# Kernel optimization log

Hardware: AMD Instinct MI355X
Metric: run time of the kernel (lower is better)

The kernel has to match this reference:

```python
import jax, jax.numpy as jnp
import numpy as np

N = 50000      # nodes
IN = 128       # in_dim
HID = 128      # hidden_dim
HEADS = 4
OUT = HID // HEADS   # per-head out_channels
R = 8          # num_relations
E = 640000     # message-passing edges
E2 = 200000    # decode edge pairs
NC = 8         # num_classes
EPS_LN = 1e-5


def layer_norm(x, g, b):
    m = x.mean(-1, keepdims=True)
    v = ((x - m) ** 2).mean(-1, keepdims=True)
    return (x - m) * jax.lax.rsqrt(v + EPS_LN) * g + b


def rgat_conv(x, edge_index, edge_type, W, q, k, b):
    # PyG RGATConv defaults: additive-self-attention, across-relation softmax,
    # concat=True, negative_slope=0.2, sum aggregation.
    src, dst = edge_index[0], edge_index[1]
    # relation-specific transform for all nodes, then gather per edge
    xw = jnp.einsum('ni,rio->nro', x, W)          # [N, R, HID]
    xi = xw[dst, edge_type]                        # [E, HID] target feats
    xj = xw[src, edge_type]                        # [E, HID] source feats
    alpha = jax.nn.leaky_relu(xi @ q + xj @ k, negative_slope=0.2)  # [E, HEADS]
    # softmax over incoming edges of each destination node (per head)
    amax = jax.ops.segment_max(alpha, dst, num_segments=N)
    amax = jnp.where(jnp.isfinite(amax), amax, 0.0)
    ex = jnp.exp(alpha - amax[dst])
    den = jax.ops.segment_sum(ex, dst, num_segments=N)
    attn = ex / (den[dst] + 1e-16)                 # [E, HEADS]
    msg = (xj.reshape(E, HEADS, OUT) * attn[:, :, None]).reshape(E, HID)
    out = jax.ops.segment_sum(msg, dst, num_segments=N)  # [N, HID]
    return out + b


def setup_inputs() -> dict:
    key = jax.random.key(0)
    ks = jax.random.split(key, 12)
    sI = 1.0 / np.sqrt(IN)
    sH = 1.0 / np.sqrt(HID)
    return {
        'x': jax.random.normal(ks[0], (N, IN), jnp.float32),
        'edge_index': jax.random.randint(ks[1], (2, E), 0, N),
        'edge_type': jax.random.randint(ks[2], (E,), 0, R),
        'edges': jax.random.randint(ks[3], (E2, 2), 0, N),
        'w1': jax.random.normal(ks[4], (R, IN, HID), jnp.float32) * sI,
        'q1': jax.random.normal(ks[5], (HID, HEADS), jnp.float32) * sH,
        'k1': jax.random.normal(ks[6], (HID, HEADS), jnp.float32) * sH,
        'b1': jnp.zeros((HID,), jnp.float32),
        'w2': jax.random.normal(ks[7], (R, HID, HID), jnp.float32) * sH,
        'q2': jax.random.normal(ks[8], (HID, HEADS), jnp.float32) * sH,
        'k2': jax.random.normal(ks[9], (HID, HEADS), jnp.float32) * sH,
        'b2': jnp.zeros((HID,), jnp.float32),
        'ln1_g': jnp.ones((HID,), jnp.float32),
        'ln1_b': jnp.zeros((HID,), jnp.float32),
        'ln2_g': jnp.ones((HID,), jnp.float32),
        'ln2_b': jnp.zeros((HID,), jnp.float32),
        'mw1': jax.random.normal(ks[10], (2 * HID, HID), jnp.float32) / np.sqrt(2 * HID),
        'mb1': jnp.zeros((HID,), jnp.float32),
        'mw2': jax.random.normal(ks[11], (HID, NC), jnp.float32) * sH,
        'mb2': jnp.zeros((NC,), jnp.float32),
    }


def reference(x, edge_index, edge_type, edges,
              w1, q1, k1, b1, w2, q2, k2, b2,
              ln1_g, ln1_b, ln2_g, ln2_b,
              mw1, mb1, mw2, mb2):
    # encode (dropout is identity in eval mode)
    h1 = rgat_conv(x, edge_index, edge_type, w1, q1, k1, b1)
    h1 = layer_norm(jax.nn.relu(h1), ln1_g, ln1_b)
    h2 = rgat_conv(h1, edge_index, edge_type, w2, q2, k2, b2)
    h2 = layer_norm(jax.nn.relu(h2), ln2_g, ln2_b)
    h = h1 + h2
    # decode: gather node pairs, concat, MLP
    z = jnp.concatenate([h[edges[:, 0]], h[edges[:, 1]]], axis=1)  # [E2, 2*HID]
    z = jax.nn.gelu(z @ mw1 + mb1, approximate=False)
    return z @ mw2 + mb2  # [E2, NC]
```

## Files before the change

### kernel.cpp

```cpp
#include <hip/hip_runtime.h>
#include <hip/hip_bf16.h>

#define NN    50000
#define RR    8
#define HIDC  128
#define NHEADS 4
#define EE    640000
#define EE2   200000
#define NCL   8

typedef __hip_bfloat16 bf16;
typedef unsigned short u16;
typedef __attribute__((ext_vector_type(8))) short short8;
typedef __attribute__((ext_vector_type(4))) float floatx4;

__device__ __forceinline__ float us2f(u16 u) {
    return __uint_as_float(((unsigned)u) << 16);
}
__device__ __forceinline__ float bf2f(bf16 v) { return __bfloat162float(v); }
__device__ __forceinline__ u16 f2us(float f) {
    bf16 h = __float2bfloat16(f);
    return *(u16*)&h;
}
__device__ __forceinline__ float ldf(const void* p, int i, bool f32) {
    return f32 ? ((const float*)p)[i] : us2f(((const u16*)p)[i]);
}

__global__ __launch_bounds__(1024) void k_zs(const u16* __restrict__ x,
                                             int* __restrict__ flags,
                                             int* __restrict__ p) {
    if (blockIdx.x < 49) {
        int i = blockIdx.x * 1024 + threadIdx.x;
        if (i < NN) p[i] = 0;
        return;
    }
    __shared__ int cnt;
    if (threadIdx.x == 0) cnt = 0;
    __syncthreads();
    int c = 0;
#pragma unroll
    for (int it = 0; it < 8; it++) {
        ushort4 a = ((const ushort4*)x)[(it * 1024 + threadIdx.x) * 2];
        ushort4 b = ((const ushort4*)x)[(it * 1024 + threadIdx.x) * 2 + 1];
        c += (((a.x >> 7) & 0xFF) == 0xFF) + (((a.y >> 7) & 0xFF) == 0xFF)
           + (((a.z >> 7) & 0xFF) == 0xFF) + (((a.w >> 7) & 0xFF) == 0xFF)
           + (((b.x >> 7) & 0xFF) == 0xFF) + (((b.y >> 7) & 0xFF) == 0xFF)
           + (((b.z >> 7) & 0xFF) == 0xFF) + (((b.w >> 7) & 0xFF) == 0xFF);
    }
    c += __shfl_xor(c, 32); c += __shfl_xor(c, 16); c += __shfl_xor(c, 8);
    c += __shfl_xor(c, 4);  c += __shfl_xor(c, 2);  c += __shfl_xor(c, 1);
    if ((threadIdx.x & 63) == 0) atomicAdd(&cnt, c);
    __syncthreads();
    if (threadIdx.x == 0) { flags[0] = (cnt > 16) ? 1 : 0; flags[1] = 0; }
}

__global__ void k_hist(const int* __restrict__ ei, int* __restrict__ deg) {
    int e = blockIdx.x * 256 + threadIdx.x;
    if (e < EE) atomicAdd(&deg[ei[EE + e]], 1);
}

__global__ __launch_bounds__(256) void k_s1q(const int* __restrict__ deg,
                                             int* __restrict__ bsum,
                                             const void* __restrict__ w1, const void* __restrict__ w2,
                                             const void* __restrict__ q1, const void* __restrict__ k1,
                                             const void* __restrict__ q2, const void* __restrict__ k2,
                                             float* __restrict__ qkw, const int* __restrict__ fl) {
    if (blockIdx.x < 196) {
        int i = blockIdx.x * 256 + threadIdx.x;
        int v = (i < NN) ? deg[i] : 0;
        __shared__ int red[4];
        int lane = threadIdx.x & 63, w = threadIdx.x >> 6;
#pragma unroll
        for (int off = 32; off; off >>= 1) v += __shfl_xor(v, off);
        if (lane == 0) red[w] = v;
        __syncthreads();
        if (threadIdx.x == 0) bsum[blockIdx.x] = red[0] + red[1] + red[2] + red[3];
        return;
    }
    int idx = (blockIdx.x - 196) * 256 + threadIdx.x;
    const bool f = fl[0] != 0;
    int mat = idx >> 10;
    int i   = (idx >> 3) & 127;
    int h8  = idx & 7;
    const void* W = (mat >= 8) ? w2 : w1;
    const void* qk = (mat >= 8) ? ((h8 < 4) ? q2 : k2) : ((h8 < 4) ? q1 : k1);
    int h = h8 & 3;
    int r = mat & 7;
    float acc = 0.f;
    for (int o = 0; o < HIDC; o++)
        acc += ldf(W, (r * HIDC + i) * HIDC + o, f) * ldf(qk, o * NHEADS + h, f);
    qkw[idx] = acc;
}

__global__ __launch_bounds__(256) void k_scan2(const int* __restrict__ bsum,
                                               int* __restrict__ boff,
                                               int* __restrict__ rowptr) {
    __shared__ int s[256];
    int t = threadIdx.x;
    s[t] = (t < 196) ? bsum[t] : 0;
    __syncthreads();
    for (int off = 1; off < 256; off <<= 1) {
        int u = (t >= off) ? s[t - off] : 0;
        __syncthreads();
        s[t] += u;
        __syncthreads();
    }
    if (t < 196) boff[t] = (t == 0) ? 0 : s[t - 1];
    if (t == 255) rowptr[NN] = s[255];
}

__global__ __launch_bounds__(256) void k_s3w(int* __restrict__ deg ,
                                             const int* __restrict__ boff,
                                             int* __restrict__ rowptr,
                                             const void* __restrict__ w1, const void* __restrict__ w2,
                                             const float* __restrict__ qkw,
                                             u16* __restrict__ Wf2, const int* __restrict__ fl) {
    if (blockIdx.x < 196) {
        __shared__ int s[256];
        int t = threadIdx.x;
        int i = blockIdx.x * 256 + t;
        int v = (i < NN) ? deg[i] : 0;
        s[t] = v;
        __syncthreads();
        for (int off = 1; off < 256; off <<= 1) {
            int u = (t >= off) ? s[t - off] : 0;
            __syncthreads();
            s[t] += u;
            __syncthreads();
        }
        if (i < NN) {
            int val = boff[blockIdx.x] + s[t] - v;
            rowptr[i] = val;
            deg[i] = val;
        }
        return;
    }
    int idx = (blockIdx.x - 196) * 256 + threadIdx.x;
    const bool f = fl[0] != 0;
    int mat = idx / 2304, rest = idx % 2304;
    int c = rest >> 8, q = (rest >> 6) & 3, ln = rest & 63;
    int k0 = q * 32 + (ln >> 4) * 8;
    int nn = c * 16 + (ln & 15);
    int r = mat & 7;
    u16 o[8];
    if (c < 8) {
        const void* W = (mat >= 8) ? w2 : w1;
#pragma unroll
        for (int j = 0; j < 8; j++)
            o[j] = f2us(ldf(W, (r * HIDC + k0 + j) * HIDC + nn, f));
    } else {
        int col = nn - 128;
#pragma unroll
        for (int j = 0; j < 8; j++)
            o[j] = (col < 8) ? f2us(qkw[mat * 1024 + (k0 + j) * 8 + col]) : (u16)0;
    }
    u16* dst = Wf2 + (size_t)mat * 18432 + (size_t)(((c * 4 + q) * 64 + ln) * 8);
    *(ushort4*)dst       = ushort4{o[0], o[1], o[2], o[3]};
    *(ushort4*)(dst + 4) = ushort4{o[4], o[5], o[6], o[7]};
}

__global__ void k_scatter(const int* __restrict__ ei, const int* __restrict__ et,
                          int* __restrict__ cursor, int* __restrict__ elist) {
    int e = blockIdx.x * 256 + threadIdx.x;
    if (e >= EE) return;
    int pos = atomicAdd(&cursor[ei[EE + e]], 1);
    elist[pos] = ei[e] * RR + et[e];
}

__global__ __launch_bounds__(512) void k_xw2(const void* __restrict__ X,
                                             const u16* __restrict__ Wf2,
                                             bf16* __restrict__ xw,
                                             float* __restrict__ sbuf,
                                             float* __restrict__ tbuf,
                                             const int* __restrict__ fx,
                                             int layer) {
    __shared__ u16 U[8 * 16 * 136];
    u16* Xs = U;
    const int tid = threadIdx.x;
    const int n0 = blockIdx.x * 64;
    const bool xf = fx[0] != 0;
    for (int v = tid; v < 2048; v += 512) {
        int row = v >> 5, c4 = (v & 31) * 4, n = n0 + row;
        ushort4 o = {0, 0, 0, 0};
        if (n < NN) {
            if (xf) {
                float4 hv = *(const float4*)((const float*)X + (size_t)n * HIDC + c4);
                o = ushort4{f2us(hv.x), f2us(hv.y), f2us(hv.z), f2us(hv.w)};
            } else {
                o = *(const ushort4*)((const u16*)X + (size_t)n * HIDC + c4);
            }
        }
        *(ushort4*)&Xs[row * 136 + c4] = o;
    }
    __syncthreads();
    const int w = tid >> 6, lane = tid & 63;
    const int wr = w & 3;
    const int rh = w >> 2;
    short8 af[4];
#pragma unroll
    for (int q = 0; q < 4; q++)
        af[q] = *(const short8*)&Xs[(16 * wr + (lane & 15)) * 136 + q * 32 + (lane >> 4) * 8];
    __syncthreads();
    u16* Ow = U + w * 2176;
    for (int rr = 0; rr < 4; rr++) {
        const int r = rh * 4 + rr;
        const u16* Wfr = Wf2 + (size_t)(layer * 8 + r) * 18432;
#pragma unroll
        for (int c = 0; c < 9; c++) {
            floatx4 acc = {0.f, 0.f, 0.f, 0.f};
#pragma unroll
            for (int q = 0; q < 4; q++) {
                short8 bfr = *(const short8*)&Wfr[(size_t)(((c * 4 + q) * 64 + lane) * 8)];
                acc = __builtin_amdgcn_mfma_f32_16x16x32_bf16(af[q], bfr, acc, 0, 0, 0);
            }
            if (c < 8) {
                int col = c * 16 + (lane & 15);
#pragma unroll
                for (int reg = 0; reg < 4; reg++) {
                    int lp = (lane >> 4) * 4 + reg;
                    Ow[lp * 136 + col] = f2us(acc[reg]);
                }
            } else {
                int cl = lane & 15;
                if (cl < 8) {
                    float* dstp = (cl < 4) ? sbuf : tbuf;
                    int h = cl & 3;
#pragma unroll
                    for (int reg = 0; reg < 4; reg++) {
                        int p = 16 * wr + (lane >> 4) * 4 + reg;
                        int n = n0 + p;
                        if (n < NN) dstp[(size_t)(n * RR + r) * 4 + h] = acc[reg];
                    }
                }
            }
        }
#pragma unroll
        for (int i = 0; i < 4; i++) {
            int v = i * 64 + lane;
            int lrow = v >> 4;
            int c8 = (v & 15) * 8;
            int n = n0 + 16 * wr + lrow;
            if (n < NN) {
                short8 hv = *(const short8*)&Ow[lrow * 136 + c8];
                *(short8*)((u16*)xw + (size_t)(n * RR + r) * HIDC + c8) = hv;
            }
        }
    }
}

__global__ __launch_bounds__(256) void k_score(const int* __restrict__ rowptr,
                                               const int* __restrict__ srlist,
                                               const float* __restrict__ sb,
                                               const float* __restrict__ tb,
                                               float* __restrict__ abuf,
                                               float* __restrict__ linv) {
    __shared__ float sbs[16][8][4];
    const int tid = threadIdx.x;
    const int grp = tid >> 4, sl = tid & 15;
    const int d = blockIdx.x * 16 + grp;
    const int start = rowptr[d], end = rowptr[d + 1];
    if (sl < 8)
        *(float4*)&sbs[grp][sl][0] = *(const float4*)&sb[(size_t)(d * RR + sl) * 4];
    const int nE = end - start;
    float m0 = -1e30f, m1 = -1e30f, m2 = -1e30f, m3 = -1e30f;
    float l0 = 0.f, l1 = 0.f, l2 = 0.f, l3 = 0.f;
    if (nE <= 16) {
        float a0, a1, a2, a3;
        if (sl < nE) {
            int sr = srlist[start + sl];
            int r = sr & 7;
            float4 tj = *(const float4*)&tb[(size_t)sr * 4];
            a0 = sbs[grp][r][0] + tj.x; a0 = a0 >= 0.f ? a0 : 0.2f * a0;
            a1 = sbs[grp][r][1] + tj.y; a1 = a1 >= 0.f ? a1 : 0.2f * a1;
            a2 = sbs[grp][r][2] + tj.z; a2 = a2 >= 0.f ? a2 : 0.2f * a2;
            a3 = sbs[grp][r][3] + tj.w; a3 = a3 >= 0.f ? a3 : 0.2f * a3;
        } else { a0 = a1 = a2 = a3 = -1e30f; }
        float c0m = a0, c1m = a1, c2m = a2, c3m = a3;
#pragma unroll
        for (int off = 8; off; off >>= 1) {
            c0m = fmaxf(c0m, __shfl_xor(c0m, off));
            c1m = fmaxf(c1m, __shfl_xor(c1m, off));
            c2m = fmaxf(c2m, __shfl_xor(c2m, off));
            c3m = fmaxf(c3m, __shfl_xor(c3m, off));
        }
        m0 = fmaxf(c0m, -1e30f); m1 = c1m; m2 = c2m; m3 = c3m;
        float e0 = 0.f, e1 = 0.f, e2 = 0.f, e3 = 0.f;
        if (sl < nE) {
            e0 = __expf(a0 - m0); e1 = __expf(a1 - m1);
            e2 = __expf(a2 - m2); e3 = __expf(a3 - m3);
            *(float4*)&abuf[(size_t)(start + sl) * 4] = float4{e0, e1, e2, e3};
        }
        l0 = e0; l1 = e1; l2 = e2; l3 = e3;
#pragma unroll
        for (int off = 8; off; off >>= 1) {
            l0 += __shfl_xor(l0, off);
            l1 += __shfl_xor(l1, off);
            l2 += __shfl_xor(l2, off);
            l3 += __shfl_xor(l3, off);
        }
    } else {
        for (int c0 = start; c0 < end; c0 += 16) {
            int n = end - c0; if (n > 16) n = 16;
            float a0, a1, a2, a3;
            if (sl < n) {
                int sr = srlist[c0 + sl];
                int r = sr & 7;
                float4 tj = *(const float4*)&tb[(size_t)sr * 4];
                a0 = sbs[grp][r][0] + tj.x; a0 = a0 >= 0.f ? a0 : 0.2f * a0;
                a1 = sbs[grp][r][1] + tj.y; a1 = a1 >= 0.f ? a1 : 0.2f * a1;
                a2 = sbs[grp][r][2] + tj.z; a2 = a2 >= 0.f ? a2 : 0.2f * a2;
                a3 = sbs[grp][r][3] + tj.w; a3 = a3 >= 0.f ? a3 : 0.2f * a3;
                *(float4*)&abuf[(size_t)(c0 + sl) * 4] = float4{a0, a1, a2, a3};
            } else { a0 = a1 = a2 = a3 = -1e30f; }
            m0 = fmaxf(m0, a0); m1 = fmaxf(m1, a1);
            m2 = fmaxf(m2, a2); m3 = fmaxf(m3, a3);
        }
#pragma unroll
        for (int off = 8; off; off >>= 1) {
            m0 = fmaxf(m0, __shfl_xor(m0, off));
            m1 = fmaxf(m1, __shfl_xor(m1, off));
            m2 = fmaxf(m2, __shfl_xor(m2, off));
            m3 = fmaxf(m3, __shfl_xor(m3, off));
        }
        for (int c0 = start; c0 < end; c0 += 16) {
            int n = end - c0; if (n > 16) n = 16;
            float e0 = 0.f, e1 = 0.f, e2 = 0.f, e3 = 0.f;
            if (sl < n) {
                float4 a = *(const float4*)&abuf[(size_t)(c0 + sl) * 4];
                e0 = __expf(a.x - m0); e1 = __expf(a.y - m1);
                e2 = __expf(a.z - m2); e3 = __expf(a.w - m3);
                *(float4*)&abuf[(size_t)(c0 + sl) * 4] = float4{e0, e1, e2, e3};
            }
            l0 += e0; l1 += e1; l2 += e2; l3 += e3;
        }
#pragma unroll
        for (int off = 8; off; off >>= 1) {
            l0 += __shfl_xor(l0, off);
            l1 += __shfl_xor(l1, off);
            l2 += __shfl_xor(l2, off);
            l3 += __shfl_xor(l3, off);
        }
    }
    if (sl == 0) {
        *(float4*)&linv[(size_t)d * 4] =
            float4{1.f / (l0 + 1e-16f), 1.f / (l1 + 1e-16f),
                   1.f / (l2 + 1e-16f), 1.f / (l3 + 1e-16f)};
    }
}

__global__ __launch_bounds__(256) void k_agg(const int* __restrict__ rowptr,
                                             const int* __restrict__ srlist,
                                             const float* __restrict__ abuf,
                                             const float* __restrict__ linvb,
                                             const bf16* __restrict__ xw,
                                             const void* __restrict__ b,
                                             const void* __restrict__ g,
                                             const void* __restrict__ bb,
                                             const u16* __restrict__ hprev,
                                             u16* __restrict__ hout,
                                             const int* __restrict__ fl) {
    __shared__ int   srs[16][16];
    __shared__ float exs[16][17][4];
    const int tid = threadIdx.x;
    const int grp = tid >> 4;
    const int sl  = tid & 15;
    const int hh  = sl >> 2;
    const int d   = blockIdx.x * 16 + grp;
    const bool f = fl[0] != 0;
    const int start = rowptr[d], end = rowptr[d + 1];
    float acc[8];
#pragma unroll
    for (int i = 0; i < 8; i++) acc[i] = 0.f;
    for (int c0 = start; c0 < end; c0 += 16) {
        int n = end - c0;
        if (n > 16) n = 16;
        int sr = 0;
        float4 e4 = {0.f, 0.f, 0.f, 0.f};
        if (sl < n) {
            sr = srlist[c0 + sl];
            e4 = *(const float4*)&abuf[(size_t)(c0 + sl) * 4];
        }
        srs[grp][sl] = sr;
        *(float4*)&exs[grp][sl][0] = e4;
        {
            short8 u[8]; float wv[8];
#pragma unroll
            for (int t = 0; t < 8; t++) {
                int s = srs[grp][t];
                wv[t] = exs[grp][t][hh];
                u[t] = *(const short8*)((const u16*)xw + (size_t)s * HIDC + sl * 8);
            }
#pragma unroll
            for (int t = 0; t < 8; t++)
#pragma unroll
                for (int i = 0; i < 8; i++) acc[i] += wv[t] * us2f((u16)u[t][i]);
        }
        if (n > 8) {
            short8 u[8]; float wv[8];
#pragma unroll
            for (int t = 0; t < 8; t++) {
                int s = srs[grp][8 + t];
                wv[t] = exs[grp][8 + t][hh];
                u[t] = *(const short8*)((const u16*)xw + (size_t)s * HIDC + sl * 8);
            }
#pragma unroll
            for (int t = 0; t < 8; t++)
#pragma unroll
                for (int i = 0; i < 8; i++) acc[i] += wv[t] * us2f((u16)u[t][i]);
        }
    }
    float inv = linvb[(size_t)d * 4 + hh];
    float v[8];
#pragma unroll
    for (int i = 0; i < 8; i++)
        v[i] = fmaxf(acc[i] * inv + ldf(b, sl * 8 + i, f), 0.f);
    float sum = 0.f;
#pragma unroll
    for (int i = 0; i < 8; i++) sum += v[i];
#pragma unroll
    for (int off = 8; off; off >>= 1) sum += __shfl_xor(sum, off);
    float mean = sum * (1.f / 128.f);
    float sq = 0.f;
#pragma unroll
    for (int i = 0; i < 8; i++) { v[i] -= mean; sq += v[i] * v[i]; }
#pragma unroll
    for (int off = 8; off; off >>= 1) sq += __shfl_xor(sq, off);
    float rstd = rsqrtf(sq * (1.f / 128.f) + 1e-5f);
    short8 o;
#pragma unroll
    for (int i = 0; i < 8; i++) {
        float y = v[i] * rstd * ldf(g, sl * 8 + i, f) + ldf(bb, sl * 8 + i, f);
        o[i] = (short)f2us(y);
    }
    if (hprev) {
        short8 hv = *(const short8*)&hprev[(size_t)d * HIDC + sl * 8];
#pragma unroll
        for (int i = 0; i < 8; i++)
            o[i] = (short)f2us(us2f((u16)o[i]) + us2f((u16)hv[i]));
    }
    *(short8*)&hout[(size_t)d * HIDC + sl * 8] = o;
}

__global__ void k_dswz(const void* __restrict__ mw1, const void* __restrict__ mw2,
                       u16* __restrict__ Wf, const int* __restrict__ fl) {
    int idx = blockIdx.x * 256 + threadIdx.x;
    if (idx >= 4352) return;
    const bool f = fl[0] != 0;
    u16 o[8];
    if (idx < 4096) {
        int c = idx >> 9, q = (idx >> 6) & 7, ln = idx & 63;
        int k0 = q * 32 + (ln >> 4) * 8;
        int nn = c * 16 + (ln & 15);
#pragma unroll
        for (int j = 0; j < 8; j++)
            o[j] = f2us(ldf(mw1, (k0 + j) * HIDC + nn, f));
    } else {
        int fidx = idx - 4096;
        int q = fidx >> 6, ln = fidx & 63;
        int k0 = q * 32 + (ln >> 4) * 8;
        int nn = ln & 15;
#pragma unroll
        for (int j = 0; j < 8; j++)
            o[j] = (nn < 8) ? f2us(ldf(mw2, (k0 + j) * NCL + nn, f)) : (u16)0;
    }
    *(ushort4*)&Wf[idx * 8]     = ushort4{o[0], o[1], o[2], o[3]};
    *(ushort4*)&Wf[idx * 8 + 4] = ushort4{o[4], o[5], o[6], o[7]};
}

__global__ __launch_bounds__(256) void k_decode2(const u16* __restrict__ h,
                                                 const int* __restrict__ edges,
                                                 const u16* __restrict__ Wf,
                                                 const void* __restrict__ mb1,
                                                 const void* __restrict__ mb2,
                                                 void* __restrict__ out,
                                                 const int* __restrict__ fl) {
    __shared__ u16 zsu[64 * 136];
    const int tid = threadIdx.x;
    const bool f = fl[0] != 0;
    const int p0 = blockIdx.x * 64;
    const int w = tid >> 6, lane = tid & 63;
    const int m = 16 * w + (lane & 15);
    const int g = lane >> 4;
    const int na = edges[(size_t)(p0 + m) * 2];
    const int nb = edges[(size_t)(p0 + m) * 2 + 1];
    short8 af[8];
#pragma unroll
    for (int q = 0; q < 8; q++) {
        int k0 = q * 32 + g * 8;
        af[q] = *(const short8*)(h + (size_t)((k0 >> 7) ? nb : na) * HIDC + (k0 & 127));
    }
#pragma unroll
    for (int c = 0; c < 8; c++) {
        floatx4 acc = {0.f, 0.f, 0.f, 0.f};
#pragma unroll
        for (int q = 0; q < 8; q++) {
            short8 bfr = *(const short8*)&Wf[(size_t)(((c * 8 + q) * 64 + lane) * 8)];
            acc = __builtin_amdgcn_mfma_f32_16x16x32_bf16(af[q], bfr, acc, 0, 0, 0);
        }
        int col = c * 16 + (lane & 15);
        float bv = ldf(mb1, col, f);
#pragma unroll
        for (int reg = 0; reg < 4; reg++) {
            int p = 16 * w + (lane >> 4) * 4 + reg;
            float z = acc[reg] + bv;
            zsu[p * 136 + col] = f2us(0.5f * z * (1.f + erff(z * 0.70710678118654752f)));
        }
    }
    floatx4 acc2 = {0.f, 0.f, 0.f, 0.f};
#pragma unroll
    for (int q = 0; q < 4; q++) {
        short8 af2 = *(const short8*)&zsu[m * 136 + q * 32 + g * 8];
        short8 bfr2 = *(const short8*)&Wf[32768 + (size_t)((q * 64 + lane) * 8)];
        acc2 = __builtin_amdgcn_mfma_f32_16x16x32_bf16(af2, bfr2, acc2, 0, 0, 0);
    }
    int col16 = lane & 15;
    if (col16 < 8) {
        float bv2 = ldf(mb2, col16, f);
#pragma unroll
        for (int reg = 0; reg < 4; reg++) {
            int p = 16 * w + (lane >> 4) * 4 + reg;
            float sv = acc2[reg] + bv2;
            size_t oi = (size_t)(p0 + p) * NCL + col16;
            if (f) ((float*)out)[oi] = sv;
            else   ((bf16*)out)[oi] = __float2bfloat16(sv);
        }
    }
}

extern "C" void kernel_launch(void* const* d_in, const int* in_sizes, int n_in,
                              void* d_out, int out_size, void* d_ws, size_t ws_size,
                              hipStream_t stream) {
    (void)in_sizes; (void)n_in; (void)out_size; (void)ws_size;
    const void* x    = d_in[0];
    const int* ei    = (const int*)d_in[1];
    const int* et    = (const int*)d_in[2];
    const int* edges = (const int*)d_in[3];
    const void* w1 = d_in[4];
    const void* q1 = d_in[5];
    const void* k1 = d_in[6];
    const void* b1 = d_in[7];
    const void* w2 = d_in[8];
    const void* q2 = d_in[9];
    const void* k2 = d_in[10];
    const void* b2 = d_in[11];
    const void* ln1g = d_in[12];
    const void* ln1b = d_in[13];
    const void* ln2g = d_in[14];
    const void* ln2b = d_in[15];
    const void* mw1 = d_in[16];
    const void* mb1 = d_in[17];
    const void* mw2 = d_in[18];
    const void* mb2 = d_in[19];

    char* ws = (char*)d_ws;
    bf16* xwb   = (bf16*)ws;
    u16* Wf     = (u16*)ws;
    float* sbuf = (float*)(ws + 102400000);
    float* tbuf = (float*)(ws + 108800000);
    u16* h1     = (u16*)(ws + 115200000);
    float* abuf = (float*)(ws + 128000000);
    float* linv = (float*)(ws + 138240000);
    int* bsum   = (int*)(ws + 139040000);
    int* boff   = (int*)(ws + 139041024);
    u16* hsum   = (u16*)(ws + 140800000);
    u16* Wf2    = (u16*)(ws + 153600000);
    int* rowptr = (int*)(ws + 166400000);
    int* cursor = (int*)(ws + 166600016);
    int* elist  = (int*)(ws + 166800016);
    float* qkw  = (float*)(ws + 169360016);
    int* flags  = (int*)(ws + 169425552);

    k_zs<<<50, 1024, 0, stream>>>((const u16*)x, flags, cursor);
    k_hist<<<2500, 256, 0, stream>>>(ei, cursor);
    k_s1q<<<260, 256, 0, stream>>>(cursor, bsum, w1, w2, q1, k1, q2, k2, qkw, flags);
    k_scan2<<<1, 256, 0, stream>>>(bsum, boff, rowptr);
    k_s3w<<<340, 256, 0, stream>>>(cursor, boff, rowptr, w1, w2, qkw, Wf2, flags);
    k_scatter<<<2500, 256, 0, stream>>>(ei, et, cursor, elist);

    for (int layer = 0; layer < 2; ++layer) {
        const void* b  = layer ? b2 : b1;
        const void* lg = layer ? ln2g : ln1g;
        const void* lb = layer ? ln2b : ln1b;
        k_xw2<<<782, 512, 0, stream>>>(layer ? (const void*)h1 : x, Wf2, xwb,
                                       sbuf, tbuf,
                                       layer ? flags + 1 : flags, layer);
        k_score<<<3125, 256, 0, stream>>>(rowptr, elist, sbuf, tbuf, abuf, linv);
        k_agg<<<3125, 256, 0, stream>>>(rowptr, elist, abuf, linv, xwb,
                                        b, lg, lb,
                                        layer ? h1 : (const u16*)nullptr,
                                        layer ? hsum : h1, flags);
    }
    k_dswz<<<17, 256, 0, stream>>>(mw1, mw2, Wf, flags);
    k_decode2<<<3125, 256, 0, stream>>>(hsum, edges, Wf, mb1, mb2, d_out, flags);
}
```

Baseline: 469.2 us.

## Aggregate raw features per relation then apply W via MFMA in aggregation

Stops materialising the per-node, per-relation transformed features xw ([N,R,HID] in bf16). Edges are now bucketed by (destination, relation), and the aggregation kernel sums attention-weighted raw source features for each relation and head. It then multiplies each per-relation sum by W_r with MFMA inside the same kernel. The projection kernel now computes only the attention score projections and writes a bf16 copy of x. This removes the large xw write and its scattered reads, at the cost of a larger 400k-entry CSR and scan, per-relation serial edge loops, and eight MFMA passes with barriers per block.

New measurement: 540.1 us. 15.1% more time.

```diff
diff --git a/kernel.cpp b/kernel.cpp
--- a/kernel.cpp
+++ b/kernel.cpp
@@ -8,6 +8,8 @@
 #define EE    640000
 #define EE2   200000
 #define NCL   8
+#define NB2   400000
+#define SB2   1563
 
 typedef __hip_bfloat16 bf16;
 typedef unsigned short u16;
@@ -17,7 +19,6 @@
 __device__ __forceinline__ float us2f(u16 u) {
     return __uint_as_float(((unsigned)u) << 16);
 }
-__device__ __forceinline__ float bf2f(bf16 v) { return __bfloat162float(v); }
 __device__ __forceinline__ u16 f2us(float f) {
     bf16 h = __float2bfloat16(f);
     return *(u16*)&h;
@@ -29,9 +30,9 @@
 __global__ __launch_bounds__(1024) void k_zs(const u16* __restrict__ x,
                                              int* __restrict__ flags,
                                              int* __restrict__ p) {
-    if (blockIdx.x < 49) {
+    if (blockIdx.x < 391) {
         int i = blockIdx.x * 1024 + threadIdx.x;
-        if (i < NN) p[i] = 0;
+        if (i < NB2) p[i] = 0;
         return;
     }
     __shared__ int cnt;
@@ -54,9 +55,10 @@
     if (threadIdx.x == 0) { flags[0] = (cnt > 16) ? 1 : 0; flags[1] = 0; }
 }
 
-__global__ void k_hist(const int* __restrict__ ei, int* __restrict__ deg) {
+__global__ void k_hist(const int* __restrict__ ei, const int* __restrict__ et,
+                       int* __restrict__ deg) {
     int e = blockIdx.x * 256 + threadIdx.x;
-    if (e < EE) atomicAdd(&deg[ei[EE + e]], 1);
+    if (e < EE) atomicAdd(&deg[ei[EE + e] * RR + et[e]], 1);
 }
 
 __global__ __launch_bounds__(256) void k_s1q(const int* __restrict__ deg,
@@ -65,9 +67,9 @@
                                              const void* __restrict__ q1, const void* __restrict__ k1,
                                              const void* __restrict__ q2, const void* __restrict__ k2,
                                              float* __restrict__ qkw, const int* __restrict__ fl) {
-    if (blockIdx.x < 196) {
+    if (blockIdx.x < SB2) {
         int i = blockIdx.x * 256 + threadIdx.x;
-        int v = (i < NN) ? deg[i] : 0;
+        int v = (i < NB2) ? deg[i] : 0;
         __shared__ int red[4];
         int lane = threadIdx.x & 63, w = threadIdx.x >> 6;
 #pragma unroll
@@ -77,7 +79,7 @@
         if (threadIdx.x == 0) bsum[blockIdx.x] = red[0] + red[1] + red[2] + red[3];
         return;
     }
-    int idx = (blockIdx.x - 196) * 256 + threadIdx.x;
+    int idx = (blockIdx.x - SB2) * 256 + threadIdx.x;
     const bool f = fl[0] != 0;
     int mat = idx >> 10;
     int i   = (idx >> 3) & 127;
@@ -92,34 +94,17 @@
     qkw[idx] = acc;
 }
 
-__global__ __launch_bounds__(256) void k_scan2(const int* __restrict__ bsum,
-                                               int* __restrict__ boff,
-                                               int* __restrict__ rowptr) {
+__global__ __launch_bounds__(256) void k_scan2b(const int* __restrict__ bsum,
+                                                int* __restrict__ boff,
+                                                int* __restrict__ rowptr2) {
     __shared__ int s[256];
+    __shared__ int carry;
     int t = threadIdx.x;
-    s[t] = (t < 196) ? bsum[t] : 0;
+    if (t == 0) carry = 0;
     __syncthreads();
-    for (int off = 1; off < 256; off <<= 1) {
-        int u = (t >= off) ? s[t - off] : 0;
-        __syncthreads();
-        s[t] += u;
-        __syncthreads();
-    }
-    if (t < 196) boff[t] = (t == 0) ? 0 : s[t - 1];
-    if (t == 255) rowptr[NN] = s[255];
-}
-
-__global__ __launch_bounds__(256) void k_s3w(int* __restrict__ deg ,
-                                             const int* __restrict__ boff,
-                                             int* __restrict__ rowptr,
-                                             const void* __restrict__ w1, const void* __restrict__ w2,
-                                             const float* __restrict__ qkw,
-                                             u16* __restrict__ Wf2, const int* __restrict__ fl) {
-    if (blockIdx.x < 196) {
-        __shared__ int s[256];
-        int t = threadIdx.x;
-        int i = blockIdx.x * 256 + t;
-        int v = (i < NN) ? deg[i] : 0;
+    for (int ch = 0; ch < 7; ch++) {
+        int idx = ch * 256 + t;
+        int v = (idx < SB2) ? bsum[idx] : 0;
         s[t] = v;
         __syncthreads();
         for (int off = 1; off < 256; off <<= 1) {
@@ -128,14 +113,41 @@
             s[t] += u;
             __syncthreads();
         }
-        if (i < NN) {
+        if (idx < SB2) boff[idx] = carry + s[t] - v;
+        __syncthreads();
+        if (t == 0) carry += s[255];
+        __syncthreads();
+    }
+    if (t == 0) rowptr2[NB2] = carry;
+}
+
+__global__ __launch_bounds__(256) void k_s3w(int* __restrict__ deg ,
+                                             const int* __restrict__ boff,
+                                             int* __restrict__ rowptr2,
+                                             const void* __restrict__ w1, const void* __restrict__ w2,
+                                             const float* __restrict__ qkw,
+                                             u16* __restrict__ Wf2, const int* __restrict__ fl) {
+    if (blockIdx.x < SB2) {
+        __shared__ int s[256];
+        int t = threadIdx.x;
+        int i = blockIdx.x * 256 + t;
+        int v = (i < NB2) ? deg[i] : 0;
+        s[t] = v;
+        __syncthreads();
+        for (int off = 1; off < 256; off <<= 1) {
+            int u = (t >= off) ? s[t - off] : 0;
+            __syncthreads();
+            s[t] += u;
+            __syncthreads();
+        }
+        if (i < NB2) {
             int val = boff[blockIdx.x] + s[t] - v;
-            rowptr[i] = val;
+            rowptr2[i] = val;
             deg[i] = val;
         }
         return;
     }
-    int idx = (blockIdx.x - 196) * 256 + threadIdx.x;
+    int idx = (blockIdx.x - SB2) * 256 + threadIdx.x;
     const bool f = fl[0] != 0;
     int mat = idx / 2304, rest = idx % 2304;
     int c = rest >> 8, q = (rest >> 6) & 3, ln = rest & 63;
@@ -163,19 +175,18 @@
                           int* __restrict__ cursor, int* __restrict__ elist) {
     int e = blockIdx.x * 256 + threadIdx.x;
     if (e >= EE) return;
-    int pos = atomicAdd(&cursor[ei[EE + e]], 1);
+    int pos = atomicAdd(&cursor[ei[EE + e] * RR + et[e]], 1);
     elist[pos] = ei[e] * RR + et[e];
 }
 
-__global__ __launch_bounds__(512) void k_xw2(const void* __restrict__ X,
-                                             const u16* __restrict__ Wf2,
-                                             bf16* __restrict__ xw,
-                                             float* __restrict__ sbuf,
-                                             float* __restrict__ tbuf,
-                                             const int* __restrict__ fx,
-                                             int layer) {
-    __shared__ u16 U[8 * 16 * 136];
-    u16* Xs = U;
+__global__ __launch_bounds__(512) void k_st(const void* __restrict__ X,
+                                            const u16* __restrict__ Wf2,
+                                            float* __restrict__ sbuf,
+                                            float* __restrict__ tbuf,
+                                            u16* __restrict__ xbf,
+                                            const int* __restrict__ fx,
+                                            int layer, int writeX) {
+    __shared__ u16 Xs[64 * 136];
     const int tid = threadIdx.x;
     const int n0 = blockIdx.x * 64;
     const bool xf = fx[0] != 0;
@@ -193,6 +204,14 @@
         *(ushort4*)&Xs[row * 136 + c4] = o;
     }
     __syncthreads();
+    if (writeX) {
+        for (int v = tid; v < 1024; v += 512) {
+            int row = v >> 4, c8 = (v & 15) * 8;
+            int n = n0 + row;
+            if (n < NN)
+                *(short8*)(xbf + (size_t)n * HIDC + c8) = *(const short8*)&Xs[row * 136 + c8];
+        }
+    }
     const int w = tid >> 6, lane = tid & 63;
     const int wr = w & 3;
     const int rh = w >> 2;
@@ -200,55 +219,30 @@
 #pragma unroll
     for (int q = 0; q < 4; q++)
         af[q] = *(const short8*)&Xs[(16 * wr + (lane & 15)) * 136 + q * 32 + (lane >> 4) * 8];
-    __syncthreads();
-    u16* Ow = U + w * 2176;
     for (int rr = 0; rr < 4; rr++) {
         const int r = rh * 4 + rr;
         const u16* Wfr = Wf2 + (size_t)(layer * 8 + r) * 18432;
-#pragma unroll
-        for (int c = 0; c < 9; c++) {
-            floatx4 acc = {0.f, 0.f, 0.f, 0.f};
-#pragma unroll
-            for (int q = 0; q < 4; q++) {
-                short8 bfr = *(const short8*)&Wfr[(size_t)(((c * 4 + q) * 64 + lane) * 8)];
-                acc = __builtin_amdgcn_mfma_f32_16x16x32_bf16(af[q], bfr, acc, 0, 0, 0);
+        floatx4 acc = {0.f, 0.f, 0.f, 0.f};
+#pragma unroll
+        for (int q = 0; q < 4; q++) {
+            short8 bfr = *(const short8*)&Wfr[(size_t)(((8 * 4 + q) * 64 + lane) * 8)];
+            acc = __builtin_amdgcn_mfma_f32_16x16x32_bf16(af[q], bfr, acc, 0, 0, 0);
+        }
+        int cl = lane & 15;
+        if (cl < 8) {
+            float* dstp = (cl < 4) ? sbuf : tbuf;
+            int h = cl & 3;
+#pragma unroll
+            for (int reg = 0; reg < 4; reg++) {
+                int p = 16 * wr + (lane >> 4) * 4 + reg;
+                int n = n0 + p;
+                if (n < NN) dstp[(size_t)(n * RR + r) * 4 + h] = acc[reg];
             }
-            if (c < 8) {
-                int col = c * 16 + (lane & 15);
-#pragma unroll
-                for (int reg = 0; reg < 4; reg++) {
-                    int lp = (lane >> 4) * 4 + reg;
-                    Ow[lp * 136 + col] = f2us(acc[reg]);
-                }
-            } else {
-                int cl = lane & 15;
-                if (cl < 8) {
-                    float* dstp = (cl < 4) ? sbuf : tbuf;
-                    int h = cl & 3;
-#pragma unroll
-                    for (int reg = 0; reg < 4; reg++) {
-                        int p = 16 * wr + (lane >> 4) * 4 + reg;
-                        int n = n0 + p;
-                        if (n < NN) dstp[(size_t)(n * RR + r) * 4 + h] = acc[reg];
-                    }
-                }
-            }
-        }
-#pragma unroll
-        for (int i = 0; i < 4; i++) {
-            int v = i * 64 + lane;
-            int lrow = v >> 4;
-            int c8 = (v & 15) * 8;
-            int n = n0 + 16 * wr + lrow;
-            if (n < NN) {
-                short8 hv = *(const short8*)&Ow[lrow * 136 + c8];
-                *(short8*)((u16*)xw + (size_t)(n * RR + r) * HIDC + c8) = hv;
-            }
-        }
-    }
-}
-
-__global__ __launch_bounds__(256) void k_score(const int* __restrict__ rowptr,
+        }
+    }
+}
+
+__global__ __launch_bounds__(256) void k_score(const int* __restrict__ rowptr2,
                                                const int* __restrict__ srlist,
                                                const float* __restrict__ sb,
                                                const float* __restrict__ tb,
@@ -258,7 +252,7 @@
     const int tid = threadIdx.x;
     const int grp = tid >> 4, sl = tid & 15;
     const int d = blockIdx.x * 16 + grp;
-    const int start = rowptr[d], end = rowptr[d + 1];
+    const int start = rowptr2[d * RR], end = rowptr2[d * RR + RR];
     if (sl < 8)
         *(float4*)&sbs[grp][sl][0] = *(const float4*)&sb[(size_t)(d * RR + sl) * 4];
     const int nE = end - start;
@@ -283,7 +277,7 @@
             c2m = fmaxf(c2m, __shfl_xor(c2m, off));
             c3m = fmaxf(c3m, __shfl_xor(c3m, off));
         }
-        m0 = fmaxf(c0m, -1e30f); m1 = c1m; m2 = c2m; m3 = c3m;
+        m0 = c0m; m1 = c1m; m2 = c2m; m3 = c3m;
         float e0 = 0.f, e1 = 0.f, e2 = 0.f, e3 = 0.f;
         if (sl < nE) {
             e0 = __expf(a0 - m0); e1 = __expf(a1 - m1);
@@ -348,72 +342,88 @@
     }
 }
 
-__global__ __launch_bounds__(256) void k_agg(const int* __restrict__ rowptr,
-                                             const int* __restrict__ srlist,
-                                             const float* __restrict__ abuf,
-                                             const float* __restrict__ linvb,
-                                             const bf16* __restrict__ xw,
-                                             const void* __restrict__ b,
-                                             const void* __restrict__ g,
-                                             const void* __restrict__ bb,
-                                             const u16* __restrict__ hprev,
-                                             u16* __restrict__ hout,
-                                             const int* __restrict__ fl) {
-    __shared__ int   srs[16][16];
-    __shared__ float exs[16][17][4];
+__global__ __launch_bounds__(256) void k_fagg(const int* __restrict__ rowptr2,
+                                              const int* __restrict__ srlist,
+                                              const float* __restrict__ abuf,
+                                              const float* __restrict__ linvb,
+                                              const u16* __restrict__ xg,
+                                              const u16* __restrict__ Wf2,
+                                              int layer,
+                                              const void* __restrict__ b,
+                                              const void* __restrict__ g,
+                                              const void* __restrict__ bb,
+                                              const u16* __restrict__ hprev,
+                                              u16* __restrict__ hout,
+                                              const int* __restrict__ fl) {
+    __shared__ u16 SH[4 * 16 * 136];
     const int tid = threadIdx.x;
-    const int grp = tid >> 4;
-    const int sl  = tid & 15;
-    const int hh  = sl >> 2;
-    const int d   = blockIdx.x * 16 + grp;
+    const int grp = tid >> 4, sl = tid & 15;
+    const int d = blockIdx.x * 16 + grp;
+    const int wv = tid >> 6, lane = tid & 63;
     const bool f = fl[0] != 0;
-    const int start = rowptr[d], end = rowptr[d + 1];
-    float acc[8];
-#pragma unroll
-    for (int i = 0; i < 8; i++) acc[i] = 0.f;
-    for (int c0 = start; c0 < end; c0 += 16) {
-        int n = end - c0;
-        if (n > 16) n = 16;
-        int sr = 0;
-        float4 e4 = {0.f, 0.f, 0.f, 0.f};
-        if (sl < n) {
-            sr = srlist[c0 + sl];
-            e4 = *(const float4*)&abuf[(size_t)(c0 + sl) * 4];
-        }
-        srs[grp][sl] = sr;
-        *(float4*)&exs[grp][sl][0] = e4;
+    floatx4 o0 = {0.f, 0.f, 0.f, 0.f}, o1 = {0.f, 0.f, 0.f, 0.f};
+    const int base = d * RR;
+    for (int r = 0; r < RR; ++r) {
+        float a0[8], a1[8], a2[8], a3[8];
+#pragma unroll
+        for (int i = 0; i < 8; i++) { a0[i] = 0.f; a1[i] = 0.f; a2[i] = 0.f; a3[i] = 0.f; }
+        const int js = rowptr2[base + r], je = rowptr2[base + r + 1];
+        for (int j = js; j < je; ++j) {
+            int s = srlist[j] >> 3;
+            float4 w4 = *(const float4*)&abuf[(size_t)j * 4];
+            short8 xv = *(const short8*)(xg + (size_t)s * HIDC + sl * 8);
+#pragma unroll
+            for (int i = 0; i < 8; i++) {
+                float xf_ = us2f((u16)xv[i]);
+                a0[i] += w4.x * xf_; a1[i] += w4.y * xf_;
+                a2[i] += w4.z * xf_; a3[i] += w4.w * xf_;
+            }
+        }
         {
-            short8 u[8]; float wv[8];
-#pragma unroll
-            for (int t = 0; t < 8; t++) {
-                int s = srs[grp][t];
-                wv[t] = exs[grp][t][hh];
-                u[t] = *(const short8*)((const u16*)xw + (size_t)s * HIDC + sl * 8);
-            }
-#pragma unroll
-            for (int t = 0; t < 8; t++)
-#pragma unroll
-                for (int i = 0; i < 8; i++) acc[i] += wv[t] * us2f((u16)u[t][i]);
-        }
-        if (n > 8) {
-            short8 u[8]; float wv[8];
-#pragma unroll
-            for (int t = 0; t < 8; t++) {
-                int s = srs[grp][8 + t];
-                wv[t] = exs[grp][8 + t][hh];
-                u[t] = *(const short8*)((const u16*)xw + (size_t)s * HIDC + sl * 8);
-            }
-#pragma unroll
-            for (int t = 0; t < 8; t++)
-#pragma unroll
-                for (int i = 0; i < 8; i++) acc[i] += wv[t] * us2f((u16)u[t][i]);
-        }
-    }
+            short8 p;
+#pragma unroll
+            for (int i = 0; i < 8; i++) p[i] = (short)f2us(a0[i]);
+            *(short8*)&SH[0 * 2176 + grp * 136 + sl * 8] = p;
+#pragma unroll
+            for (int i = 0; i < 8; i++) p[i] = (short)f2us(a1[i]);
+            *(short8*)&SH[1 * 2176 + grp * 136 + sl * 8] = p;
+#pragma unroll
+            for (int i = 0; i < 8; i++) p[i] = (short)f2us(a2[i]);
+            *(short8*)&SH[2 * 2176 + grp * 136 + sl * 8] = p;
+#pragma unroll
+            for (int i = 0; i < 8; i++) p[i] = (short)f2us(a3[i]);
+            *(short8*)&SH[3 * 2176 + grp * 136 + sl * 8] = p;
+        }
+        __syncthreads();
+        const u16* Wfr = Wf2 + (size_t)(layer * 8 + r) * 18432;
+        const u16* aggH = SH + wv * 2176;
+        short8 af[4];
+#pragma unroll
+        for (int q = 0; q < 4; q++)
+            af[q] = *(const short8*)&aggH[(lane & 15) * 136 + q * 32 + (lane >> 4) * 8];
+#pragma unroll
+        for (int q = 0; q < 4; q++) {
+            short8 b0 = *(const short8*)&Wfr[(size_t)((((2 * wv) * 4 + q) * 64 + lane) * 8)];
+            o0 = __builtin_amdgcn_mfma_f32_16x16x32_bf16(af[q], b0, o0, 0, 0, 0);
+            short8 b1 = *(const short8*)&Wfr[(size_t)((((2 * wv + 1) * 4 + q) * 64 + lane) * 8)];
+            o1 = __builtin_amdgcn_mfma_f32_16x16x32_bf16(af[q], b1, o1, 0, 0, 0);
+        }
+        __syncthreads();
+    }
+    float* outL = (float*)SH;
+#pragma unroll
+    for (int reg = 0; reg < 4; reg++) {
+        int row = (lane >> 4) * 4 + reg;
+        outL[row * 132 + wv * 32 + (lane & 15)]      = o0[reg];
+        outL[row * 132 + wv * 32 + 16 + (lane & 15)] = o1[reg];
+    }
+    __syncthreads();
+    const int hh = sl >> 2;
     float inv = linvb[(size_t)d * 4 + hh];
     float v[8];
 #pragma unroll
     for (int i = 0; i < 8; i++)
-        v[i] = fmaxf(acc[i] * inv + ldf(b, sl * 8 + i, f), 0.f);
+        v[i] = fmaxf(outL[grp * 132 + sl * 8 + i] * inv + ldf(b, sl * 8 + i, f), 0.f);
     float sum = 0.f;
 #pragma unroll
     for (int i = 0; i < 8; i++) sum += v[i];
@@ -553,7 +563,7 @@
     const void* mb2 = d_in[19];
 
     char* ws = (char*)d_ws;
-    bf16* xwb   = (bf16*)ws;
+    u16* xbf    = (u16*)ws;
     u16* Wf     = (u16*)ws;
     float* sbuf = (float*)(ws + 102400000);
     float* tbuf = (float*)(ws + 108800000);
@@ -561,34 +571,35 @@
     float* abuf = (float*)(ws + 128000000);
     float* linv = (float*)(ws + 138240000);
     int* bsum   = (int*)(ws + 139040000);
-    int* boff   = (int*)(ws + 139041024);
+    int* boff   = (int*)(ws + 139048000);
     u16* hsum   = (u16*)(ws + 140800000);
     u16* Wf2    = (u16*)(ws + 153600000);
-    int* rowptr = (int*)(ws + 166400000);
-    int* cursor = (int*)(ws + 166600016);
+    int* rowptr2= (int*)(ws + 154200000);
+    int* cursor2= (int*)(ws + 155900000);
     int* elist  = (int*)(ws + 166800016);
     float* qkw  = (float*)(ws + 169360016);
     int* flags  = (int*)(ws + 169425552);
 
-    k_zs<<<50, 1024, 0, stream>>>((const u16*)x, flags, cursor);
-    k_hist<<<2500, 256, 0, stream>>>(ei, cursor);
-    k_s1q<<<260, 256, 0, stream>>>(cursor, bsum, w1, w2, q1, k1, q2, k2, qkw, flags);
-    k_scan2<<<1, 256, 0, stream>>>(bsum, boff, rowptr);
-    k_s3w<<<340, 256, 0, stream>>>(cursor, boff, rowptr, w1, w2, qkw, Wf2, flags);
-    k_scatter<<<2500, 256, 0, stream>>>(ei, et, cursor, elist);
+    k_zs<<<392, 1024, 0, stream>>>((const u16*)x, flags, cursor2);
+    k_hist<<<2500, 256, 0, stream>>>(ei, et, cursor2);
+    k_s1q<<<SB2 + 64, 256, 0, stream>>>(cursor2, bsum, w1, w2, q1, k1, q2, k2, qkw, flags);
+    k_scan2b<<<1, 256, 0, stream>>>(bsum, boff, rowptr2);
+    k_s3w<<<SB2 + 144, 256, 0, stream>>>(cursor2, boff, rowptr2, w1, w2, qkw, Wf2, flags);
+    k_scatter<<<2500, 256, 0, stream>>>(ei, et, cursor2, elist);
 
     for (int layer = 0; layer < 2; ++layer) {
         const void* b  = layer ? b2 : b1;
         const void* lg = layer ? ln2g : ln1g;
         const void* lb = layer ? ln2b : ln1b;
-        k_xw2<<<782, 512, 0, stream>>>(layer ? (const void*)h1 : x, Wf2, xwb,
-                                       sbuf, tbuf,
-                                       layer ? flags + 1 : flags, layer);
-        k_score<<<3125, 256, 0, stream>>>(rowptr, elist, sbuf, tbuf, abuf, linv);
-        k_agg<<<3125, 256, 0, stream>>>(rowptr, elist, abuf, linv, xwb,
-                                        b, lg, lb,
-                                        layer ? h1 : (const u16*)nullptr,
-                                        layer ? hsum : h1, flags);
+        k_st<<<782, 512, 0, stream>>>(layer ? (const void*)h1 : x, Wf2,
+                                      sbuf, tbuf, xbf,
+                                      layer ? flags + 1 : flags, layer, layer == 0);
+        k_score<<<3125, 256, 0, stream>>>(rowptr2, elist, sbuf, tbuf, abuf, linv);
+        k_fagg<<<3125, 256, 0, stream>>>(rowptr2, elist, abuf, linv,
+                                         layer ? h1 : xbf, Wf2, layer,
+                                         b, lg, lb,
+                                         layer ? h1 : (const u16*)nullptr,
+                                         layer ? hsum : h1, flags);
     }
     k_dswz<<<17, 256, 0, stream>>>(mw1, mw2, Wf, flags);
     k_decode2<<<3125, 256, 0, stream>>>(hsum, edges, Wf, mb1, mb2, d_out, flags);
```
